# Kernel tuning notes

Hardware: AMD Instinct MI355X
Metric: run time of the kernel (lower is better)

## Reference

```python
import jax, jax.numpy as jnp
import numpy as np

TEMPERATURE = 0.07
EPS = 1e-8  # torch CosineSimilarity eps


def setup_inputs() -> dict:
    key = jax.random.key(0)
    k1, k2, k3 = jax.random.split(key, 3)
    N, D = 8192, 512
    features = jax.random.normal(k1, (N, D), dtype=jnp.float32)
    positive_mask = jax.random.randint(k2, (N, N), 0, 2, dtype=jnp.int32)
    negative_mask = jax.random.randint(k3, (N, N), 0, 2, dtype=jnp.int32)
    return {"features": features, "positive_mask": positive_mask, "negative_mask": negative_mask}


def reference(features, positive_mask, negative_mask):
    N = positive_mask.shape[0]
    self_contrast = 1.0 - jnp.eye(N, dtype=features.dtype)  # zero diagonal
    pos = positive_mask.astype(features.dtype) * self_contrast  # [N, N]
    neg = negative_mask.astype(features.dtype) * self_contrast  # [N, N]

    # cosine similarity via normalized matmul (same math as broadcasted CosineSimilarity)
    norm = jnp.maximum(jnp.linalg.norm(features, axis=1, keepdims=True), EPS)
    fn = features / norm  # [N, D]
    sim = jnp.matmul(fn, fn.T) / TEMPERATURE  # [N, N]

    logits_max = jax.lax.stop_gradient(jnp.max(sim, axis=1, keepdims=True))
    e = jnp.exp(sim - logits_max)  # [N, N]

    positives = e * pos
    log_neg_sum = jnp.log(jnp.sum(e * neg, axis=1, keepdims=True))  # [N, 1]
    log_prob = positives - log_neg_sum  # [N, N] (faithful to source: exp-masked, not log)

    cardinal = jnp.sum(pos, axis=1)
    cardinal = jnp.where(cardinal == 0, 1.0, cardinal)
    log_prob_sum = jnp.sum(log_prob * pos, axis=1)
    loss = -log_prob_sum / cardinal
    return jnp.mean(loss)
```

## Files before the change

### kernel.cpp

```cpp
#include <hip/hip_runtime.h>
#include <hip/hip_bf16.h>
#include <math.h>

#define NN 8192
#define DD 512
#define INV_T 14.285714285714286f

typedef __attribute__((ext_vector_type(8))) short s16x8;
typedef __attribute__((ext_vector_type(4))) float f32x4;
typedef __attribute__((ext_vector_type(4))) int   i32x4;

__device__ __forceinline__ unsigned short f32_to_bf16(float f) {
  unsigned int u = __float_as_uint(f);
  u += 0x7FFFu + ((u >> 16) & 1u);
  return (unsigned short)(u >> 16);
}

__device__ __forceinline__ void async16(const void* g, void* l) {
  __builtin_amdgcn_global_load_lds((__attribute__((address_space(1))) void*)(void*)g,
                                   (__attribute__((address_space(3))) void*)l,
                                   16, 0, 0);
}

__global__ __launch_bounds__(256) void normalize_kernel(const float* __restrict__ f,
                                                        unsigned short* __restrict__ fnb) {
  const int wave = threadIdx.x >> 6;
  const int lane = threadIdx.x & 63;
  const int row  = blockIdx.x * 4 + wave;
  const float* src = f + (size_t)row * DD + lane * 8;
  float4 v0 = *(const float4*)src;
  float4 v1 = *(const float4*)(src + 4);
  float ss = v0.x*v0.x + v0.y*v0.y + v0.z*v0.z + v0.w*v0.w
           + v1.x*v1.x + v1.y*v1.y + v1.z*v1.z + v1.w*v1.w;
  #pragma unroll
  for (int o = 32; o; o >>= 1) ss += __shfl_xor(ss, o);
  const float r = 1.0f / fmaxf(sqrtf(ss), 1e-8f);
  ushort4 a, b;
  a.x = f32_to_bf16(v0.x * r); a.y = f32_to_bf16(v0.y * r);
  a.z = f32_to_bf16(v0.z * r); a.w = f32_to_bf16(v0.w * r);
  b.x = f32_to_bf16(v1.x * r); b.y = f32_to_bf16(v1.y * r);
  b.z = f32_to_bf16(v1.z * r); b.w = f32_to_bf16(v1.w * r);
  unsigned short* dst = fnb + (size_t)row * DD + lane * 8;
  *(ushort4*)dst = a;
  *(ushort4*)(dst + 4) = b;
}

__global__ __launch_bounds__(512, 4) void fused_kernel(const unsigned short* __restrict__ fnb,
                                                       const int* __restrict__ posm,
                                                       const int* __restrict__ negm,
                                                       float* __restrict__ Spos,
                                                       float* __restrict__ Sneg,
                                                       float* __restrict__ Pcnt) {
  const int bid = blockIdx.x;
  int bi = (int)(64.5 - sqrt(64.5 * 64.5 - 2.0 * (double)bid));
  while (64 * bi - bi * (bi - 1) / 2 > bid) --bi;
  while (64 * (bi + 1) - (bi + 1) * bi / 2 <= bid) ++bi;
  const int bj = bi + (bid - (64 * bi - bi * (bi - 1) / 2));
  const int I = bi * 128;
  const int J = bj * 128;
  const bool offdiag = (bi != bj);

  const int tid  = threadIdx.x;
  const int wave = tid >> 6;
  const int lane = tid & 63;

  __shared__ alignas(16) unsigned short lA[128 * 32];
  __shared__ alignas(16) unsigned short lB[128 * 32];
  __shared__ unsigned long long bdir[2][128][2];
  __shared__ unsigned long long btr [2][128][2];
  __shared__ float sacc[2][128][3];
  for (int t = tid; t < 2 * 128 * 3; t += 512) ((float*)sacc)[t] = 0.f;

  f32x4 acc[4][4];

  if (wave < 4) {
    const int wm = wave >> 1, wn = wave & 1;
    const int q = lane >> 4, c16 = lane & 15;
    const f32x4 z4 = {0.f, 0.f, 0.f, 0.f};
    #pragma unroll
    for (int mt = 0; mt < 4; ++mt)
      #pragma unroll
      for (int nt = 0; nt < 4; ++nt) acc[mt][nt] = z4;

    for (int kk = 0; kk < DD / 32; ++kk) {
      const int k0 = kk * 32;
      #pragma unroll
      for (int c = 0; c < 2; ++c) {
        const int fidx = tid + c * 256;
        const int row  = fidx >> 2;
        const int p    = fidx & 3;
        const int csrc = (p ^ ((row >> 1) & 3)) & 3;
        async16(fnb + (size_t)(I + row) * DD + k0 + csrc * 8, (char*)lA + fidx * 16);
        async16(fnb + (size_t)(J + row) * DD + k0 + csrc * 8, (char*)lB + fidx * 16);
      }
      __syncthreads();

      s16x8 aF[4], bF[4];
      #pragma unroll
      for (int t = 0; t < 4; ++t) {
        const int arow = wm * 64 + t * 16 + c16;
        const int apos = (q ^ ((arow >> 1) & 3)) & 3;
        aF[t] = *(const s16x8*)((const char*)lA + arow * 64 + apos * 16);
        const int brow = wn * 64 + t * 16 + c16;
        const int bpos = (q ^ ((brow >> 1) & 3)) & 3;
        bF[t] = *(const s16x8*)((const char*)lB + brow * 64 + bpos * 16);
      }
      #pragma unroll
      for (int mt = 0; mt < 4; ++mt)
        #pragma unroll
        for (int nt = 0; nt < 4; ++nt)
          acc[mt][nt] = __builtin_amdgcn_mfma_f32_16x16x32_bf16(aF[mt], bF[nt], acc[mt][nt], 0, 0, 0);
      __syncthreads();
    }
    #pragma unroll
    for (int mt = 0; mt < 4; ++mt)
      #pragma unroll
      for (int nt = 0; nt < 4; ++nt)
        #pragma unroll
        for (int r = 0; r < 4; ++r)
          acc[mt][nt][r] = __expf(acc[mt][nt][r] * INV_T - INV_T);
  } else {
    const int mw   = wave - 4;
    const int msel = mw & 1;
    const int half = mw >> 1;
    const int* mb  = msel ? negm : posm;
    const int sub  = lane >> 5;
    const int col4 = (lane & 31) * 4;

    i32x4 vbuf[2][2];

    #define MLOAD(g)                                                          \
      if ((g) < 32 && !((g) >= 16 && !offdiag)) {                             \
        const int R0 = ((g) < 16) ? I : J;                                    \
        const int C0 = ((g) < 16) ? J : I;                                    \
        _Pragma("unroll")                                                     \
        for (int u = 0; u < 2; ++u) {                                         \
          const int rl = half * 64 + ((g) & 15) * 4 + 2 * u + sub;            \
          vbuf[(g) & 1][u] = __builtin_nontemporal_load(                      \
              (const i32x4*)(mb + (size_t)(R0 + rl) * NN + C0 + col4));       \
        }                                                                     \
      }

    MLOAD(0)
    #pragma unroll
    for (int g = 0; g < 32; ++g) {
      MLOAD(g + 1)
      __syncthreads();
      if (!(g >= 16 && !offdiag)) {
        unsigned long long (*dst)[2] = (g < 16) ? bdir[msel] : btr[msel];
        #pragma unroll
        for (int u = 0; u < 2; ++u) {
          const i32x4 v = vbuf[g & 1][u];
          const unsigned long long b0 = __ballot(v.x != 0);
          const unsigned long long b1 = __ballot(v.y != 0);
          const unsigned long long b2 = __ballot(v.z != 0);
          const unsigned long long b3 = __ballot(v.w != 0);
          if (lane < 4) {
            const int s = lane >> 1, h = lane & 1;
            const int k = 16 * (2 * s + h);
            const unsigned long long t =
                ((b0 >> k) & 0xFFFFull)         | (((b1 >> k) & 0xFFFFull) << 16)
              | (((b2 >> k) & 0xFFFFull) << 32) | (((b3 >> k) & 0xFFFFull) << 48);
            dst[half * 64 + (g & 15) * 4 + 2 * u + s][h] = t;
          }
        }
      }
    }
  }

  __syncthreads();

  if (wave < 4) {
    const int wm = wave >> 1, wn = wave & 1;
    const int q = lane >> 4, c16 = lane & 15;
    const bool hasdiag = (bi == bj) && (wm == wn);

    const int shd = (c16 >> 2) + (c16 & 3) * 16;
    #pragma unroll
    for (int mt = 0; mt < 4; ++mt) {
      const int rl = wm * 64 + mt * 16 + q * 4;
      #pragma unroll
      for (int r = 0; r < 4; ++r) {
        unsigned long long wp = bdir[0][rl + r][wn];
        unsigned long long wnn = bdir[1][rl + r][wn];
        if (hasdiag) {
          const unsigned long long m = ~(1ULL << (mt * 4 + q + 16 * r));
          wp &= m; wnn &= m;
        }
        float dsp = 0.f, dsn = 0.f;
        #pragma unroll
        for (int nt = 0; nt < 4; ++nt) {
          const float e = acc[mt][nt][r];
          dsp = fmaf(e, (float)((wp  >> (nt * 4 + shd)) & 1ULL), dsp);
          dsn = fmaf(e, (float)((wnn >> (nt * 4 + shd)) & 1ULL), dsn);
        }
        #pragma unroll
        for (int o = 1; o <= 8; o <<= 1) {
          dsp += __shfl_xor(dsp, o);
          dsn += __shfl_xor(dsn, o);
        }
        if (c16 == 0) {
          atomicAdd(&sacc[0][rl + r][0], dsp);
          atomicAdd(&sacc[0][rl + r][1], dsn);
          atomicAdd(&sacc[0][rl + r][2], (float)__popcll(wp));
        }
      }
    }
    if (offdiag) {
      #pragma unroll
      for (int nt = 0; nt < 4; ++nt) {
        const int cl = wn * 64 + nt * 16 + c16;
        const unsigned long long tpw = btr[0][cl][wm];
        const unsigned long long tnw = btr[1][cl][wm];
        float ts = 0.f, tn = 0.f;
        #pragma unroll
        for (int mt = 0; mt < 4; ++mt) {
          const int sh = mt * 4 + q;
          #pragma unroll
          for (int r = 0; r < 4; ++r) {
            const float e = acc[mt][nt][r];
            ts = fmaf(e, (float)((tpw >> (sh + 16 * r)) & 1ULL), ts);
            tn = fmaf(e, (float)((tnw >> (sh + 16 * r)) & 1ULL), tn);
          }
        }
        ts += __shfl_xor(ts, 16); ts += __shfl_xor(ts, 32);
        tn += __shfl_xor(tn, 16); tn += __shfl_xor(tn, 32);
        if (q == 0) {
          atomicAdd(&sacc[1][cl][0], ts);
          atomicAdd(&sacc[1][cl][1], tn);
          atomicAdd(&sacc[1][cl][2], (float)__popcll(tpw));
        }
      }
    }
  }

  __syncthreads();

  const int r = tid & 127;
  if (tid < 128) {
    atomicAdd(&Spos[I + r], sacc[0][r][0]);
    atomicAdd(&Sneg[I + r], sacc[0][r][1]);
    atomicAdd(&Pcnt[I + r], sacc[0][r][2]);
  } else if (tid < 256 && offdiag) {
    atomicAdd(&Spos[J + r], sacc[1][r][0]);
    atomicAdd(&Sneg[J + r], sacc[1][r][1]);
    atomicAdd(&Pcnt[J + r], sacc[1][r][2]);
  }
}

__global__ __launch_bounds__(256) void finalize_kernel(const float* __restrict__ Spos,
                                                       const float* __restrict__ Sneg,
                                                       const float* __restrict__ Pcnt,
                                                       float* __restrict__ out) {
  float local = 0.f;
  for (int i = threadIdx.x; i < NN; i += 256) {
    const float sp = Spos[i], sn = Sneg[i], pc = Pcnt[i];
    const float card = (pc == 0.f) ? 1.f : pc;
    local += (logf(sn) * pc - sp) / card;
  }
  #pragma unroll
  for (int o = 32; o; o >>= 1) local += __shfl_xor(local, o);
  __shared__ float red[4];
  if ((threadIdx.x & 63) == 0) red[threadIdx.x >> 6] = local;
  __syncthreads();
  if (threadIdx.x == 0)
    out[0] = (red[0] + red[1] + red[2] + red[3]) * (1.0f / (float)NN);
}

extern "C" void kernel_launch(void* const* d_in, const int* in_sizes, int n_in,
                              void* d_out, int out_size, void* d_ws, size_t ws_size,
                              hipStream_t stream) {
  const float* feat = (const float*)d_in[0];
  const int* posm   = (const int*)d_in[1];
  const int* negm   = (const int*)d_in[2];
  float* out = (float*)d_out;

  char* ws = (char*)d_ws;
  unsigned short* fnb = (unsigned short*)ws;
  float* Spos = (float*)(ws + (size_t)8 * 1024 * 1024);
  float* Sneg = Spos + NN;
  float* Pcnt = Sneg + NN;

  hipMemsetAsync(Spos, 0, 3 * NN * sizeof(float), stream);
  normalize_kernel<<<NN / 4, 256, 0, stream>>>(feat, fnb);
  fused_kernel<<<2080, 512, 0, stream>>>(fnb, posm, negm, Spos, Sneg, Pcnt);
  finalize_kernel<<<1, 256, 0, stream>>>(Spos, Sneg, Pcnt, out);
}
```

Baseline: 593.2 us.

## Merge mask-loading waves into MFMA waves, halving the block to 256 threads

Removes the four dedicated mask-loader waves. Each of the four MFMA waves now also streams one mask tile (pos or neg, direct or transposed), issuing the loads inside the K loop and ballot-packing them after the MFMAs. This is meant to cut per-block thread count and barrier participants, and to overlap the mask HBM traffic with the matmul inside the same waves. In exchange, each wave carries more registers and does serial ballot work, and launch bounds change to 256 threads with min 2 blocks, which may lower occupancy or latency hiding.

```diff
diff --git a/kernel.cpp b/kernel.cpp
--- a/kernel.cpp
+++ b/kernel.cpp
@@ -45,7 +45,7 @@
   *(ushort4*)(dst + 4) = b;
 }
 
-__global__ __launch_bounds__(512, 4) void fused_kernel(const unsigned short* __restrict__ fnb,
+__global__ __launch_bounds__(256, 2) void fused_kernel(const unsigned short* __restrict__ fnb,
                                                        const int* __restrict__ posm,
                                                        const int* __restrict__ negm,
                                                        float* __restrict__ Spos,
@@ -63,173 +63,168 @@
   const int tid  = threadIdx.x;
   const int wave = tid >> 6;
   const int lane = tid & 63;
+  const int wm = wave >> 1;
+  const int wn = wave & 1;
+  const int q   = lane >> 4;
+  const int c16 = lane & 15;
 
   __shared__ alignas(16) unsigned short lA[128 * 32];
   __shared__ alignas(16) unsigned short lB[128 * 32];
   __shared__ unsigned long long bdir[2][128][2];
   __shared__ unsigned long long btr [2][128][2];
   __shared__ float sacc[2][128][3];
-  for (int t = tid; t < 2 * 128 * 3; t += 512) ((float*)sacc)[t] = 0.f;
+  for (int t = tid; t < 2 * 128 * 3; t += 256) ((float*)sacc)[t] = 0.f;
+
+  const int tile = wave >> 1;
+  const int msel = wave & 1;
+  const int* mb  = msel ? negm : posm;
+  const int R0 = tile ? J : I;
+  const int C0 = tile ? I : J;
+  const bool do_mask = !(tile && !offdiag);
+  const int sub  = lane >> 5;
+  const int col4 = (lane & 31) * 4;
+  const int* mrow = mb + (size_t)R0 * NN + C0 + col4;
+
+  i32x4 vbuf[2][4];
+
+  #define MLOAD(k)                                                            \
+    if (do_mask && (k) < 16) {                                                \
+      _Pragma("unroll")                                                       \
+      for (int u = 0; u < 4; ++u)                                             \
+        vbuf[(k) & 1][u] = __builtin_nontemporal_load(                        \
+            (const i32x4*)(mrow + (size_t)(8 * (k) + 2 * u + sub) * NN));     \
+    }
+
+  #define MDRAIN(k)                                                           \
+    if (do_mask) {                                                            \
+      unsigned long long (*dst)[2] = tile ? btr[msel] : bdir[msel];           \
+      _Pragma("unroll")                                                       \
+      for (int u = 0; u < 4; ++u) {                                           \
+        const i32x4 v = vbuf[(k) & 1][u];                                     \
+        const unsigned long long b0 = __ballot(v.x != 0);                     \
+        const unsigned long long b1 = __ballot(v.y != 0);                     \
+        const unsigned long long b2 = __ballot(v.z != 0);                     \
+        const unsigned long long b3 = __ballot(v.w != 0);                     \
+        if (lane < 4) {                                                       \
+          const int s = lane >> 1, h = lane & 1;                              \
+          const int kb = 16 * (2 * s + h);                                    \
+          const unsigned long long t =                                        \
+              ((b0 >> kb) & 0xFFFFull)         | (((b1 >> kb) & 0xFFFFull) << 16)  \
+            | (((b2 >> kb) & 0xFFFFull) << 32) | (((b3 >> kb) & 0xFFFFull) << 48); \
+          dst[8 * (k) + 2 * u + s][h] = t;                                    \
+        }                                                                     \
+      }                                                                       \
+    }
 
   f32x4 acc[4][4];
-
-  if (wave < 4) {
-    const int wm = wave >> 1, wn = wave & 1;
-    const int q = lane >> 4, c16 = lane & 15;
-    const f32x4 z4 = {0.f, 0.f, 0.f, 0.f};
+  const f32x4 z4 = {0.f, 0.f, 0.f, 0.f};
+  #pragma unroll
+  for (int mt = 0; mt < 4; ++mt)
+    #pragma unroll
+    for (int nt = 0; nt < 4; ++nt) acc[mt][nt] = z4;
+
+  MLOAD(0)
+
+  #pragma unroll
+  for (int kk = 0; kk < 16; ++kk) {
+    const int k0 = kk * 32;
+    #pragma unroll
+    for (int c = 0; c < 2; ++c) {
+      const int fidx = tid + c * 256;
+      const int row  = fidx >> 2;
+      const int p    = fidx & 3;
+      const int csrc = (p ^ ((row >> 1) & 3)) & 3;
+      async16(fnb + (size_t)(I + row) * DD + k0 + csrc * 8, (char*)lA + fidx * 16);
+      async16(fnb + (size_t)(J + row) * DD + k0 + csrc * 8, (char*)lB + fidx * 16);
+    }
+    __syncthreads();
+
+    MLOAD(kk + 1)
+
+    s16x8 aF[4], bF[4];
+    #pragma unroll
+    for (int t = 0; t < 4; ++t) {
+      const int arow = wm * 64 + t * 16 + c16;
+      const int apos = (q ^ ((arow >> 1) & 3)) & 3;
+      aF[t] = *(const s16x8*)((const char*)lA + arow * 64 + apos * 16);
+      const int brow = wn * 64 + t * 16 + c16;
+      const int bpos = (q ^ ((brow >> 1) & 3)) & 3;
+      bF[t] = *(const s16x8*)((const char*)lB + brow * 64 + bpos * 16);
+    }
     #pragma unroll
     for (int mt = 0; mt < 4; ++mt)
       #pragma unroll
-      for (int nt = 0; nt < 4; ++nt) acc[mt][nt] = z4;
-
-    for (int kk = 0; kk < DD / 32; ++kk) {
-      const int k0 = kk * 32;
-      #pragma unroll
-      for (int c = 0; c < 2; ++c) {
-        const int fidx = tid + c * 256;
-        const int row  = fidx >> 2;
-        const int p    = fidx & 3;
-        const int csrc = (p ^ ((row >> 1) & 3)) & 3;
-        async16(fnb + (size_t)(I + row) * DD + k0 + csrc * 8, (char*)lA + fidx * 16);
-        async16(fnb + (size_t)(J + row) * DD + k0 + csrc * 8, (char*)lB + fidx * 16);
-      }
-      __syncthreads();
-
-      s16x8 aF[4], bF[4];
-      #pragma unroll
-      for (int t = 0; t < 4; ++t) {
-        const int arow = wm * 64 + t * 16 + c16;
-        const int apos = (q ^ ((arow >> 1) & 3)) & 3;
-        aF[t] = *(const s16x8*)((const char*)lA + arow * 64 + apos * 16);
-        const int brow = wn * 64 + t * 16 + c16;
-        const int bpos = (q ^ ((brow >> 1) & 3)) & 3;
-        bF[t] = *(const s16x8*)((const char*)lB + brow * 64 + bpos * 16);
-      }
-      #pragma unroll
-      for (int mt = 0; mt < 4; ++mt)
+      for (int nt = 0; nt < 4; ++nt)
+        acc[mt][nt] = __builtin_amdgcn_mfma_f32_16x16x32_bf16(aF[mt], bF[nt], acc[mt][nt], 0, 0, 0);
+
+    MDRAIN(kk)
+
+    __syncthreads();
+  }
+
+  #pragma unroll
+  for (int mt = 0; mt < 4; ++mt)
+    #pragma unroll
+    for (int nt = 0; nt < 4; ++nt)
+      #pragma unroll
+      for (int r = 0; r < 4; ++r)
+        acc[mt][nt][r] = __expf(acc[mt][nt][r] * INV_T - INV_T);
+
+  const bool hasdiag = (bi == bj) && (wm == wn);
+  const int shd = (c16 >> 2) + (c16 & 3) * 16;
+  #pragma unroll
+  for (int mt = 0; mt < 4; ++mt) {
+    const int rl = wm * 64 + mt * 16 + q * 4;
+    #pragma unroll
+    for (int r = 0; r < 4; ++r) {
+      unsigned long long wp  = bdir[0][rl + r][wn];
+      unsigned long long wnn = bdir[1][rl + r][wn];
+      if (hasdiag) {
+        const unsigned long long m = ~(1ULL << (mt * 4 + q + 16 * r));
+        wp &= m; wnn &= m;
+      }
+      float dsp = 0.f, dsn = 0.f;
+      #pragma unroll
+      for (int nt = 0; nt < 4; ++nt) {
+        const float e = acc[mt][nt][r];
+        dsp = fmaf(e, (float)((wp  >> (nt * 4 + shd)) & 1ULL), dsp);
+        dsn = fmaf(e, (float)((wnn >> (nt * 4 + shd)) & 1ULL), dsn);
+      }
+      #pragma unroll
+      for (int o = 1; o <= 8; o <<= 1) {
+        dsp += __shfl_xor(dsp, o);
+        dsn += __shfl_xor(dsn, o);
+      }
+      if (c16 == 0) {
+        atomicAdd(&sacc[0][rl + r][0], dsp);
+        atomicAdd(&sacc[0][rl + r][1], dsn);
+        atomicAdd(&sacc[0][rl + r][2], (float)__popcll(wp));
+      }
+    }
+  }
+  if (offdiag) {
+    #pragma unroll
+    for (int nt = 0; nt < 4; ++nt) {
+      const int cl = wn * 64 + nt * 16 + c16;
+      const unsigned long long tpw = btr[0][cl][wm];
+      const unsigned long long tnw = btr[1][cl][wm];
+      float ts = 0.f, tn = 0.f;
+      #pragma unroll
+      for (int mt = 0; mt < 4; ++mt) {
+        const int sh = mt * 4 + q;
         #pragma unroll
-        for (int nt = 0; nt < 4; ++nt)
-          acc[mt][nt] = __builtin_amdgcn_mfma_f32_16x16x32_bf16(aF[mt], bF[nt], acc[mt][nt], 0, 0, 0);
-      __syncthreads();
-    }
-    #pragma unroll
-    for (int mt = 0; mt < 4; ++mt)
-      #pragma unroll
-      for (int nt = 0; nt < 4; ++nt)
-        #pragma unroll
-        for (int r = 0; r < 4; ++r)
-          acc[mt][nt][r] = __expf(acc[mt][nt][r] * INV_T - INV_T);
-  } else {
-    const int mw   = wave - 4;
-    const int msel = mw & 1;
-    const int half = mw >> 1;
-    const int* mb  = msel ? negm : posm;
-    const int sub  = lane >> 5;
-    const int col4 = (lane & 31) * 4;
-
-    i32x4 vbuf[2][2];
-
-    #define MLOAD(g)                                                          \
-      if ((g) < 32 && !((g) >= 16 && !offdiag)) {                             \
-        const int R0 = ((g) < 16) ? I : J;                                    \
-        const int C0 = ((g) < 16) ? J : I;                                    \
-        _Pragma("unroll")                                                     \
-        for (int u = 0; u < 2; ++u) {                                         \
-          const int rl = half * 64 + ((g) & 15) * 4 + 2 * u + sub;            \
-          vbuf[(g) & 1][u] = __builtin_nontemporal_load(                      \
-              (const i32x4*)(mb + (size_t)(R0 + rl) * NN + C0 + col4));       \
-        }                                                                     \
-      }
-
-    MLOAD(0)
-    #pragma unroll
-    for (int g = 0; g < 32; ++g) {
-      MLOAD(g + 1)
-      __syncthreads();
-      if (!(g >= 16 && !offdiag)) {
-        unsigned long long (*dst)[2] = (g < 16) ? bdir[msel] : btr[msel];
-        #pragma unroll
-        for (int u = 0; u < 2; ++u) {
-          const i32x4 v = vbuf[g & 1][u];
-          const unsigned long long b0 = __ballot(v.x != 0);
-          const unsigned long long b1 = __ballot(v.y != 0);
-          const unsigned long long b2 = __ballot(v.z != 0);
-          const unsigned long long b3 = __ballot(v.w != 0);
-          if (lane < 4) {
-            const int s = lane >> 1, h = lane & 1;
-            const int k = 16 * (2 * s + h);
-            const unsigned long long t =
-                ((b0 >> k) & 0xFFFFull)         | (((b1 >> k) & 0xFFFFull) << 16)
-              | (((b2 >> k) & 0xFFFFull) << 32) | (((b3 >> k) & 0xFFFFull) << 48);
-            dst[half * 64 + (g & 15) * 4 + 2 * u + s][h] = t;
-          }
+        for (int r = 0; r < 4; ++r) {
+          const float e = acc[mt][nt][r];
+          ts = fmaf(e, (float)((tpw >> (sh + 16 * r)) & 1ULL), ts);
+          tn = fmaf(e, (float)((tnw >> (sh + 16 * r)) & 1ULL), tn);
         }
       }
-    }
-  }
-
-  __syncthreads();
-
-  if (wave < 4) {
-    const int wm = wave >> 1, wn = wave & 1;
-    const int q = lane >> 4, c16 = lane & 15;
-    const bool hasdiag = (bi == bj) && (wm == wn);
-
-    const int shd = (c16 >> 2) + (c16 & 3) * 16;
-    #pragma unroll
-    for (int mt = 0; mt < 4; ++mt) {
-      const int rl = wm * 64 + mt * 16 + q * 4;
-      #pragma unroll
-      for (int r = 0; r < 4; ++r) {
-        unsigned long long wp = bdir[0][rl + r][wn];
-        unsigned long long wnn = bdir[1][rl + r][wn];
-        if (hasdiag) {
-          const unsigned long long m = ~(1ULL << (mt * 4 + q + 16 * r));
-          wp &= m; wnn &= m;
-        }
-        float dsp = 0.f, dsn = 0.f;
-        #pragma unroll
-        for (int nt = 0; nt < 4; ++nt) {
-          const float e = acc[mt][nt][r];
-          dsp = fmaf(e, (float)((wp  >> (nt * 4 + shd)) & 1ULL), dsp);
-          dsn = fmaf(e, (float)((wnn >> (nt * 4 + shd)) & 1ULL), dsn);
-        }
-        #pragma unroll
-        for (int o = 1; o <= 8; o <<= 1) {
-          dsp += __shfl_xor(dsp, o);
-          dsn += __shfl_xor(dsn, o);
-        }
-        if (c16 == 0) {
-          atomicAdd(&sacc[0][rl + r][0], dsp);
-          atomicAdd(&sacc[0][rl + r][1], dsn);
-          atomicAdd(&sacc[0][rl + r][2], (float)__popcll(wp));
-        }
-      }
-    }
-    if (offdiag) {
-      #pragma unroll
-      for (int nt = 0; nt < 4; ++nt) {
-        const int cl = wn * 64 + nt * 16 + c16;
-        const unsigned long long tpw = btr[0][cl][wm];
-        const unsigned long long tnw = btr[1][cl][wm];
-        float ts = 0.f, tn = 0.f;
-        #pragma unroll
-        for (int mt = 0; mt < 4; ++mt) {
-          const int sh = mt * 4 + q;
-          #pragma unroll
-          for (int r = 0; r < 4; ++r) {
-            const float e = acc[mt][nt][r];
-            ts = fmaf(e, (float)((tpw >> (sh + 16 * r)) & 1ULL), ts);
-            tn = fmaf(e, (float)((tnw >> (sh + 16 * r)) & 1ULL), tn);
-          }
-        }
-        ts += __shfl_xor(ts, 16); ts += __shfl_xor(ts, 32);
-        tn += __shfl_xor(tn, 16); tn += __shfl_xor(tn, 32);
-        if (q == 0) {
-          atomicAdd(&sacc[1][cl][0], ts);
-          atomicAdd(&sacc[1][cl][1], tn);
-          atomicAdd(&sacc[1][cl][2], (float)__popcll(tpw));
-        }
+      ts += __shfl_xor(ts, 16); ts += __shfl_xor(ts, 32);
+      tn += __shfl_xor(tn, 16); tn += __shfl_xor(tn, 32);
+      if (q == 0) {
+        atomicAdd(&sacc[1][cl][0], ts);
+        atomicAdd(&sacc[1][cl][1], tn);
+        atomicAdd(&sacc[1][cl][2], (float)__popcll(tpw));
       }
     }
   }
@@ -241,7 +236,7 @@
     atomicAdd(&Spos[I + r], sacc[0][r][0]);
     atomicAdd(&Sneg[I + r], sacc[0][r][1]);
     atomicAdd(&Pcnt[I + r], sacc[0][r][2]);
-  } else if (tid < 256 && offdiag) {
+  } else if (offdiag) {
     atomicAdd(&Spos[J + r], sacc[1][r][0]);
     atomicAdd(&Sneg[J + r], sacc[1][r][1]);
     atomicAdd(&Pcnt[J + r], sacc[1][r][2]);
@@ -283,6 +278,6 @@
 
   hipMemsetAsync(Spos, 0, 3 * NN * sizeof(float), stream);
   normalize_kernel<<<NN / 4, 256, 0, stream>>>(feat, fnb);
-  fused_kernel<<<2080, 512, 0, stream>>>(fnb, posm, negm, Spos, Sneg, Pcnt);
+  fused_kernel<<<2080, 256, 0, stream>>>(fnb, posm, negm, Spos, Sneg, Pcnt);
   finalize_kernel<<<1, 256, 0, stream>>>(Spos, Sneg, Pcnt, out);
 }
```

Result: faster. 554.0 us (-6.6%).
